# Kernel tuning notes

Measured on AMD Instinct MI355X. Metric: run time of the kernel, lower is better.

The kernel has to match this reference:

```python
import jax, jax.numpy as jnp
import numpy as np

EPS_NORM = 1e-12
EPS_ENT = 1e-12
TEMPERATURE = 0.5
CONTRAST_DENOM = 128.0 * 100.0


def _l2_normalize(x, axis=-1):
    n = jnp.linalg.norm(x, axis=axis, keepdims=True)
    return x / jnp.maximum(n, EPS_NORM)


def setup_inputs() -> dict:
    key0 = jax.random.key(0)
    k1, k2, k3, k4 = jax.random.split(key0, 4)
    B, L, C = 16, 2048, 512
    M = 512
    return {
        "key": jax.random.normal(k1, (B, L, C), dtype=jnp.float32),
        "query": jax.random.normal(k2, (B, L, C), dtype=jnp.float32),
        "keys": jax.random.uniform(k3, (M, C), dtype=jnp.float32),
        "values": jax.random.uniform(k4, (M, C), dtype=jnp.float32),
        "mode": 0,
    }


def reference(key, query, keys, values, mode):
    B, L, C = key.shape
    k = _l2_normalize(key.reshape(-1, C))    # [T, C]
    q = _l2_normalize(query.reshape(-1, C))  # [T, C]

    # --- gatheringLoss ---
    score = jnp.einsum('tc,mc->tm', k, keys)            # [T, M]
    # top-1 of softmax(score) == argmax(score) (softmax is monotone)
    idx = jnp.argmax(score, axis=1)                     # [T]
    nearest_values = values[idx]                        # [T, C]
    gathering_loss = jnp.mean((q - nearest_values) ** 2)

    logits = score / TEMPERATURE                        # [T, M]
    logp = jax.nn.log_softmax(logits, axis=-1)
    gathered = jnp.take_along_axis(logp, idx[:, None], axis=1)  # [T, 1]
    contrast_loss = jnp.sum(gathered) / (-CONTRAST_DENOM)

    # --- read ---
    weights = jax.nn.softmax(score, axis=-1)            # [T, M]
    # EntropyLoss: mean over rows of -sum(w * log(w + eps))
    entropy_loss = jnp.mean(-jnp.sum(weights * jnp.log(weights + EPS_ENT), axis=-1))
    read_query = weights @ values                       # [T, C]

    return (read_query.reshape(B, L, C), entropy_loss, gathering_loss,
            contrast_loss, keys, values)
```

## Files before the change

### kernel.cpp

```cpp
#include <hip/hip_runtime.h>

typedef short short8 __attribute__((ext_vector_type(8)));
typedef float floatx4 __attribute__((ext_vector_type(4)));

#define C_DIM 512
#define KQ_STRIDE 1040
#define ROWS 128

__device__ __forceinline__ unsigned short f2bf(float f) {
    unsigned u = __builtin_bit_cast(unsigned, f);
    u = u + 0x7fffu + ((u >> 16) & 1u);
    return (unsigned short)(u >> 16);
}

__device__ __forceinline__ unsigned skey(float s, int col) {
    unsigned u = __builtin_bit_cast(unsigned, s);
    u = ((int)u < 0) ? ~u : (u | 0x80000000u);
    return (u & ~0x1FFu) | (unsigned)(511 - col);
}

template <int CTRL>
__device__ __forceinline__ float dppAddF(float x) {
    int t = __builtin_amdgcn_update_dpp(0, __builtin_bit_cast(int, x), CTRL, 0xF, 0xF, true);
    return x + __builtin_bit_cast(float, t);
}
template <int CTRL>
__device__ __forceinline__ unsigned dppMaxU(unsigned x) {
    unsigned u = (unsigned)__builtin_amdgcn_update_dpp(0, (int)x, CTRL, 0xF, 0xF, true);
    return u > x ? u : x;
}
__device__ __forceinline__ float rowAdd16(float x) {
    x = dppAddF<0xB1>(x);
    x = dppAddF<0x4E>(x);
    x = dppAddF<0x124>(x);
    x = dppAddF<0x128>(x);
    return x;
}

__global__ __launch_bounds__(256) void pack_kernel(
    const float* __restrict__ keys, const float* __restrict__ values,
    unsigned short* __restrict__ keysFrag, unsigned short* __restrict__ valsFrag,
    float* __restrict__ keysOut, float* __restrict__ valsOut,
    float* __restrict__ scal) {
    int tid = blockIdx.x * 256 + threadIdx.x;
    if (tid < 65536) {
        int e  = tid & 32767;
        int l  = e & 63;
        int NT = (e >> 6) & 31;
        int kt = e >> 11;
        int li = l & 15, q4 = l >> 4;
        unsigned short tmp[8];
        if (tid < 32768) {
            const float* s = keys + (size_t)(NT * 16 + li) * C_DIM + kt * 32 + q4 * 8;
#pragma unroll
            for (int j = 0; j < 8; j++) tmp[j] = f2bf(s[j]);
            unsigned short* d = keysFrag + ((size_t)(kt * 32 + NT) * 64 + l) * 8;
            *(ushort4*)d       = make_ushort4(tmp[0], tmp[1], tmp[2], tmp[3]);
            *(ushort4*)(d + 4) = make_ushort4(tmp[4], tmp[5], tmp[6], tmp[7]);
        } else {
#pragma unroll
            for (int j = 0; j < 8; j++)
                tmp[j] = f2bf(values[(size_t)(kt * 32 + q4 * 8 + j) * C_DIM + NT * 16 + li]);
            unsigned short* d = valsFrag + ((size_t)(kt * 32 + NT) * 64 + l) * 8;
            *(ushort4*)d       = make_ushort4(tmp[0], tmp[1], tmp[2], tmp[3]);
            *(ushort4*)(d + 4) = make_ushort4(tmp[4], tmp[5], tmp[6], tmp[7]);
        }
    } else {
        int ct = tid - 65536;
        if (ct == 0) { scal[0] = 0.f; scal[1] = 0.f; scal[2] = 0.f; }
#pragma unroll
        for (int i = 0; i < 4; i++) {
            int idx = ct + i * 32768;
            if (idx < 65536) ((float4*)keysOut)[idx] = ((const float4*)keys)[idx];
            else             ((float4*)valsOut)[idx - 65536] = ((const float4*)values)[idx - 65536];
        }
    }
}

__global__ __launch_bounds__(512, 2) void fused_kernel(
    const float* __restrict__ key,
    const float* __restrict__ query,
    const unsigned short* __restrict__ keysFrag,
    const unsigned short* __restrict__ valsFrag,
    const float* __restrict__ values,
    float* __restrict__ outRQ,
    float* __restrict__ scal) {
    __shared__ char kq[ROWS * KQ_STRIDE];
    __shared__ __align__(16) float stats[8][ROWS][4];
    __shared__ float gpart[8];

    const int tid = threadIdx.x;
    const int w  = tid >> 6;
    const int l  = tid & 63;
    const int li = l & 15;
    const int q4 = l >> 4;
    const int row0 = blockIdx.x << 7;

    const float* qtb = query + (size_t)row0 * C_DIM;
    float tch0 = qtb[(tid)        * 32];
    float tch1 = qtb[(tid +  512) * 32];
    float tch2 = qtb[(tid + 1024) * 32];
    float tch3 = qtb[(tid + 1536) * 32];

#pragma unroll
    for (int it = 0; it < 4; it++) {
        int r = (w << 4) + (it << 2) + q4;
        const float4* src = (const float4*)(key + (size_t)(row0 + r) * C_DIM);
        float4 v[8];
        float ss = 0.f;
#pragma unroll
        for (int i = 0; i < 8; i++) {
            v[i] = src[i * 16 + li];
            ss += v[i].x * v[i].x + v[i].y * v[i].y + v[i].z * v[i].z + v[i].w * v[i].w;
        }
        ss = rowAdd16(ss);
        float inv = 1.0f / fmaxf(sqrtf(ss), 1e-12f);
        char* dstrow = kq + r * KQ_STRIDE;
#pragma unroll
        for (int i = 0; i < 8; i++) {
            ushort4 b = make_ushort4(f2bf(v[i].x * inv), f2bf(v[i].y * inv),
                                     f2bf(v[i].z * inv), f2bf(v[i].w * inv));
            *(ushort4*)(dstrow + i * 128 + li * 8) = b;
        }
    }
    asm volatile("" :: "v"(tch0), "v"(tch1), "v"(tch2), "v"(tch3));
    __syncthreads();

    floatx4 acc1[32];
#pragma unroll
    for (int i = 0; i < 32; i++) acc1[i] = (floatx4){0.f, 0.f, 0.f, 0.f};
    {
        const short8* kf = (const short8*)keysFrag;
        short8 bcur[4], bnxt[4];
#pragma unroll
        for (int nt = 0; nt < 4; nt++) bcur[nt] = kf[(size_t)((w * 4 + nt) * 64 + l)];
        for (int kt = 0; kt < 16; kt++) {
            if (kt < 15) {
#pragma unroll
                for (int nt = 0; nt < 4; nt++)
                    bnxt[nt] = kf[(size_t)(((kt + 1) * 32 + w * 4 + nt) * 64 + l)];
            }
            short8 a[8];
#pragma unroll
            for (int rg = 0; rg < 8; rg++)
                a[rg] = *(const short8*)(kq + (rg * 16 + li) * KQ_STRIDE + kt * 64 + q4 * 16);
#pragma unroll
            for (int rg = 0; rg < 8; rg++)
#pragma unroll
                for (int nt = 0; nt < 4; nt++)
                    acc1[rg * 4 + nt] = __builtin_amdgcn_mfma_f32_16x16x32_bf16(
                        a[rg], bcur[nt], acc1[rg * 4 + nt], 0, 0, 0);
#pragma unroll
            for (int nt = 0; nt < 4; nt++) bcur[nt] = bnxt[nt];
        }
    }

#pragma unroll
    for (int rg = 0; rg < 8; rg++) {
#pragma unroll
        for (int reg = 0; reg < 4; reg++) {
            const int colbase = (w << 6) + li;
            float s0 = acc1[rg * 4 + 0][reg];
            float s1 = acc1[rg * 4 + 1][reg];
            float s2 = acc1[rg * 4 + 2][reg];
            float s3 = acc1[rg * 4 + 3][reg];
            unsigned K  = skey(s0, colbase);
            unsigned K1 = skey(s1, colbase + 16);
            unsigned K2 = skey(s2, colbase + 32);
            unsigned K3 = skey(s3, colbase + 48);
            K = K1 > K ? K1 : K;
            K = K2 > K ? K2 : K;
            K = K3 > K ? K3 : K;
            float p0 = __expf(s0), p1 = __expf(s1), p2 = __expf(s2), p3 = __expf(s3);
            float z1 = (p0 + p1) + (p2 + p3);
            float e1 = p0 * s0 + p1 * s1 + p2 * s2 + p3 * s3;
            float z2 = p0 * p0 + p1 * p1 + p2 * p2 + p3 * p3;
            acc1[rg * 4 + 0][reg] = p0;
            acc1[rg * 4 + 1][reg] = p1;
            acc1[rg * 4 + 2][reg] = p2;
            acc1[rg * 4 + 3][reg] = p3;
            K = dppMaxU<0xB1>(K);  z1 = dppAddF<0xB1>(z1);  e1 = dppAddF<0xB1>(e1);  z2 = dppAddF<0xB1>(z2);
            K = dppMaxU<0x4E>(K);  z1 = dppAddF<0x4E>(z1);  e1 = dppAddF<0x4E>(e1);  z2 = dppAddF<0x4E>(z2);
            K = dppMaxU<0x124>(K); z1 = dppAddF<0x124>(z1); e1 = dppAddF<0x124>(e1); z2 = dppAddF<0x124>(z2);
            K = dppMaxU<0x128>(K); z1 = dppAddF<0x128>(z1); e1 = dppAddF<0x128>(e1); z2 = dppAddF<0x128>(z2);
            if (li == 0) {
                floatx4 sv;
                sv[0] = __builtin_bit_cast(float, K);
                sv[1] = z1; sv[2] = e1; sv[3] = z2;
                *(floatx4*)stats[w][rg * 16 + q4 * 4 + reg] = sv;
            }
        }
    }
    __syncthreads();

#pragma unroll
    for (int rg = 0; rg < 8; rg++) {
#pragma unroll
        for (int reg = 0; reg < 4; reg++) {
            int r = rg * 16 + q4 * 4 + reg;
#pragma unroll
            for (int nt = 0; nt < 4; nt++) {
                int col = (w << 6) + nt * 16 + li;
                *(unsigned short*)(kq + r * KQ_STRIDE + col * 2) = f2bf(acc1[rg * 4 + nt][reg]);
            }
        }
    }
    __syncthreads();

    floatx4 acc2[32];
#pragma unroll
    for (int i = 0; i < 32; i++) acc2[i] = (floatx4){0.f, 0.f, 0.f, 0.f};
    {
        const short8* vf = (const short8*)valsFrag;
        short8 bcur[4], bnxt[4];
#pragma unroll
        for (int nt = 0; nt < 4; nt++) bcur[nt] = vf[(size_t)((w * 4 + nt) * 64 + l)];
        for (int kt = 0; kt < 16; kt++) {
            if (kt < 15) {
#pragma unroll
                for (int nt = 0; nt < 4; nt++)
                    bnxt[nt] = vf[(size_t)(((kt + 1) * 32 + w * 4 + nt) * 64 + l)];
            }
            short8 a[8];
#pragma unroll
            for (int rg = 0; rg < 8; rg++)
                a[rg] = *(const short8*)(kq + (rg * 16 + li) * KQ_STRIDE + kt * 64 + q4 * 16);
#pragma unroll
            for (int rg = 0; rg < 8; rg++)
#pragma unroll
                for (int nt = 0; nt < 4; nt++)
                    acc2[rg * 4 + nt] = __builtin_amdgcn_mfma_f32_16x16x32_bf16(
                        a[rg], bcur[nt], acc2[rg * 4 + nt], 0, 0, 0);
#pragma unroll
            for (int nt = 0; nt < 4; nt++) bcur[nt] = bnxt[nt];
        }
    }

    unsigned KA, KB; float z1A, e1A, z2A, z1B, e1B, z2B;
    {
        floatx4 vA = *(const floatx4*)stats[0][l];
        floatx4 vB = *(const floatx4*)stats[0][64 + l];
        KA = __builtin_bit_cast(unsigned, vA[0]); z1A = vA[1]; e1A = vA[2]; z2A = vA[3];
        KB = __builtin_bit_cast(unsigned, vB[0]); z1B = vB[1]; e1B = vB[2]; z2B = vB[3];
#pragma unroll
        for (int p = 1; p < 8; p++) {
            floatx4 uA = *(const floatx4*)stats[p][l];
            floatx4 uB = *(const floatx4*)stats[p][64 + l];
            unsigned KoA = __builtin_bit_cast(unsigned, uA[0]);
            unsigned KoB = __builtin_bit_cast(unsigned, uB[0]);
            KA = KoA > KA ? KoA : KA; z1A += uA[1]; e1A += uA[2]; z2A += uA[3];
            KB = KoB > KB ? KoB : KB; z1B += uB[1]; e1B += uB[2]; z2B += uB[3];
        }
    }
    const float izA = 1.0f / z1A;
    const float izB = 1.0f / z1B;
    const int idxA = 511 - (int)(KA & 0x1FFu);
    const int idxB = 511 - (int)(KB & 0x1FFu);

#pragma unroll
    for (int rg = 0; rg < 8; rg++) {
#pragma unroll
        for (int reg = 0; reg < 4; reg++) {
            int r = rg * 16 + q4 * 4 + reg;
            float izr = (rg < 4) ? __shfl(izA, r & 63, 64) : __shfl(izB, r & 63, 64);
            float* orow = outRQ + (size_t)(row0 + r) * C_DIM + (w << 6) + li;
#pragma unroll
            for (int nt = 0; nt < 4; nt++) orow[nt * 16] = acc2[rg * 4 + nt][reg] * izr;
        }
    }

    float gacc = 0.f;
#pragma unroll
    for (int rr = 0; rr < 16; rr++) {
        int r = (w << 4) + rr;
        int idxr = __shfl((w < 4) ? idxA : idxB, r & 63, 64);
        const float4* qr = (const float4*)(query + (size_t)(row0 + r) * C_DIM);
        float4 a = qr[l * 2], b = qr[l * 2 + 1];
        float ss = a.x * a.x + a.y * a.y + a.z * a.z + a.w * a.w +
                   b.x * b.x + b.y * b.y + b.z * b.z + b.w * b.w;
        ss = rowAdd16(ss);
        ss += __shfl_xor(ss, 16, 64);
        ss += __shfl_xor(ss, 32, 64);
        float inv = 1.0f / fmaxf(sqrtf(ss), 1e-12f);
        const float4* vr = (const float4*)(values + (size_t)idxr * C_DIM);
        float4 va = vr[l * 2], vb = vr[l * 2 + 1];
        float d;
        d = a.x * inv - va.x; gacc += d * d;
        d = a.y * inv - va.y; gacc += d * d;
        d = a.z * inv - va.z; gacc += d * d;
        d = a.w * inv - va.w; gacc += d * d;
        d = b.x * inv - vb.x; gacc += d * d;
        d = b.y * inv - vb.y; gacc += d * d;
        d = b.z * inv - vb.z; gacc += d * d;
        d = b.w * inv - vb.w; gacc += d * d;
    }
    gacc = rowAdd16(gacc);
    gacc += __shfl_xor(gacc, 16, 64);
    gacc += __shfl_xor(gacc, 32, 64);
    if (l == 0) gpart[w] = gacc;

    if (w == 0) {
        unsigned umA = (KA >> 31) ? (KA & 0x7FFFFFFFu) : ~KA;
        unsigned umB = (KB >> 31) ? (KB & 0x7FFFFFFFu) : ~KB;
        umA &= ~0x1FFu; umB &= ~0x1FFu;
        float m1A = __builtin_bit_cast(float, umA);
        float m1B = __builtin_bit_cast(float, umB);
        float ent = (__logf(z1A) - e1A * izA) + (__logf(z1B) - e1B * izB);
        float con = (__logf(z2A) - 2.0f * m1A) + (__logf(z2B) - 2.0f * m1B);
#pragma unroll
        for (int msk = 1; msk < 64; msk <<= 1) {
            ent += __shfl_xor(ent, msk, 64);
            con += __shfl_xor(con, msk, 64);
        }
        if (l == 0) {
            atomicAdd(&scal[0], ent * (1.0f / 32768.0f));
            atomicAdd(&scal[2], con * (1.0f / 12800.0f));
        }
    }
    __syncthreads();
    if (tid == 0) {
        float s = 0.f;
#pragma unroll
        for (int i = 0; i < 8; i++) s += gpart[i];
        atomicAdd(&scal[1], s * (1.0f / (32768.0f * 512.0f)));
    }
}

extern "C" void kernel_launch(void* const* d_in, const int* in_sizes, int n_in,
                              void* d_out, int out_size, void* d_ws, size_t ws_size,
                              hipStream_t stream) {
    (void)in_sizes; (void)n_in; (void)out_size; (void)ws_size;
    const float* key    = (const float*)d_in[0];
    const float* query  = (const float*)d_in[1];
    const float* keysIn = (const float*)d_in[2];
    const float* valsIn = (const float*)d_in[3];
    float* out = (float*)d_out;

    unsigned short* keysFrag = (unsigned short*)d_ws;
    unsigned short* valsFrag = keysFrag + 512 * 512;

    float* outRQ   = out;
    float* scal    = out + 16777216;
    float* keysOut = out + 16777219;
    float* valsOut = keysOut + 262144;

    pack_kernel<<<384, 256, 0, stream>>>(keysIn, valsIn, keysFrag, valsFrag,
                                         keysOut, valsOut, scal);
    fused_kernel<<<256, 512, 0, stream>>>(key, query, keysFrag, valsFrag, valsIn, outRQ, scal);
}
```

Baseline: 235.7 us.

## Split fused kernel into score, gather and PV kernels staged through output buffer

Splits the single fused kernel into three launches: a score kernel that writes bf16 probabilities, the per-row inverse sum and the argmax index into scratch space inside the output buffer; a gather kernel that computes the gathering loss; and a PV kernel that reloads the probabilities and does the second matmul. The aim appears to be probing whether the fused kernel's phases (register pressure, serialized query gather) cost more than running them separately. In exchange it adds two launches and a round-trip of the score tile through global memory.

```diff
diff --git a/kernel.cpp b/kernel.cpp
--- a/kernel.cpp
+++ b/kernel.cpp
@@ -77,17 +77,13 @@
     }
 }
 
-__global__ __launch_bounds__(512, 2) void fused_kernel(
+__global__ __launch_bounds__(512, 2) void score_kernel(
     const float* __restrict__ key,
-    const float* __restrict__ query,
     const unsigned short* __restrict__ keysFrag,
-    const unsigned short* __restrict__ valsFrag,
-    const float* __restrict__ values,
     float* __restrict__ outRQ,
     float* __restrict__ scal) {
     __shared__ char kq[ROWS * KQ_STRIDE];
     __shared__ __align__(16) float stats[8][ROWS][4];
-    __shared__ float gpart[8];
 
     const int tid = threadIdx.x;
     const int w  = tid >> 6;
@@ -95,12 +91,7 @@
     const int li = l & 15;
     const int q4 = l >> 4;
     const int row0 = blockIdx.x << 7;
-
-    const float* qtb = query + (size_t)row0 * C_DIM;
-    float tch0 = qtb[(tid)        * 32];
-    float tch1 = qtb[(tid +  512) * 32];
-    float tch2 = qtb[(tid + 1024) * 32];
-    float tch3 = qtb[(tid + 1536) * 32];
+    char* outb = (char*)outRQ;
 
 #pragma unroll
     for (int it = 0; it < 4; it++) {
@@ -123,7 +114,6 @@
             *(ushort4*)(dstrow + i * 128 + li * 8) = b;
         }
     }
-    asm volatile("" :: "v"(tch0), "v"(tch1), "v"(tch2), "v"(tch3));
     __syncthreads();
 
     floatx4 acc1[32];
@@ -193,51 +183,8 @@
     }
     __syncthreads();
 
-#pragma unroll
-    for (int rg = 0; rg < 8; rg++) {
-#pragma unroll
-        for (int reg = 0; reg < 4; reg++) {
-            int r = rg * 16 + q4 * 4 + reg;
-#pragma unroll
-            for (int nt = 0; nt < 4; nt++) {
-                int col = (w << 6) + nt * 16 + li;
-                *(unsigned short*)(kq + r * KQ_STRIDE + col * 2) = f2bf(acc1[rg * 4 + nt][reg]);
-            }
-        }
-    }
-    __syncthreads();
-
-    floatx4 acc2[32];
-#pragma unroll
-    for (int i = 0; i < 32; i++) acc2[i] = (floatx4){0.f, 0.f, 0.f, 0.f};
-    {
-        const short8* vf = (const short8*)valsFrag;
-        short8 bcur[4], bnxt[4];
-#pragma unroll
-        for (int nt = 0; nt < 4; nt++) bcur[nt] = vf[(size_t)((w * 4 + nt) * 64 + l)];
-        for (int kt = 0; kt < 16; kt++) {
-            if (kt < 15) {
-#pragma unroll
-                for (int nt = 0; nt < 4; nt++)
-                    bnxt[nt] = vf[(size_t)(((kt + 1) * 32 + w * 4 + nt) * 64 + l)];
-            }
-            short8 a[8];
-#pragma unroll
-            for (int rg = 0; rg < 8; rg++)
-                a[rg] = *(const short8*)(kq + (rg * 16 + li) * KQ_STRIDE + kt * 64 + q4 * 16);
-#pragma unroll
-            for (int rg = 0; rg < 8; rg++)
-#pragma unroll
-                for (int nt = 0; nt < 4; nt++)
-                    acc2[rg * 4 + nt] = __builtin_amdgcn_mfma_f32_16x16x32_bf16(
-                        a[rg], bcur[nt], acc2[rg * 4 + nt], 0, 0, 0);
-#pragma unroll
-            for (int nt = 0; nt < 4; nt++) bcur[nt] = bnxt[nt];
-        }
-    }
-
-    unsigned KA, KB; float z1A, e1A, z2A, z1B, e1B, z2B;
-    {
+    if (w == 0) {
+        unsigned KA, KB; float z1A, e1A, z2A, z1B, e1B, z2B;
         floatx4 vA = *(const floatx4*)stats[0][l];
         floatx4 vB = *(const floatx4*)stats[0][64 + l];
         KA = __builtin_bit_cast(unsigned, vA[0]); z1A = vA[1]; e1A = vA[2]; z2A = vA[3];
@@ -251,30 +198,71 @@
             KA = KoA > KA ? KoA : KA; z1A += uA[1]; e1A += uA[2]; z2A += uA[3];
             KB = KoB > KB ? KoB : KB; z1B += uB[1]; e1B += uB[2]; z2B += uB[3];
         }
-    }
-    const float izA = 1.0f / z1A;
-    const float izB = 1.0f / z1B;
-    const int idxA = 511 - (int)(KA & 0x1FFu);
-    const int idxB = 511 - (int)(KB & 0x1FFu);
+        float izA = 1.0f / z1A, izB = 1.0f / z1B;
+        int idxA = 511 - (int)(KA & 0x1FFu);
+        int idxB = 511 - (int)(KB & 0x1FFu);
+        char* h0 = outb + (size_t)(row0 + l) * 2048;
+        char* h1 = outb + (size_t)(row0 + 64 + l) * 2048;
+        *(float*)h0 = izA; *(int*)(h0 + 4) = idxA;
+        *(float*)h1 = izB; *(int*)(h1 + 4) = idxB;
+        unsigned umA = (KA >> 31) ? (KA & 0x7FFFFFFFu) : ~KA;
+        unsigned umB = (KB >> 31) ? (KB & 0x7FFFFFFFu) : ~KB;
+        umA &= ~0x1FFu; umB &= ~0x1FFu;
+        float m1A = __builtin_bit_cast(float, umA);
+        float m1B = __builtin_bit_cast(float, umB);
+        float ent = (__logf(z1A) - e1A * izA) + (__logf(z1B) - e1B * izB);
+        float con = (__logf(z2A) - 2.0f * m1A) + (__logf(z2B) - 2.0f * m1B);
+#pragma unroll
+        for (int msk = 1; msk < 64; msk <<= 1) {
+            ent += __shfl_xor(ent, msk, 64);
+            con += __shfl_xor(con, msk, 64);
+        }
+        if (l == 0) {
+            atomicAdd(&scal[0], ent * (1.0f / 32768.0f));
+            atomicAdd(&scal[2], con * (1.0f / 12800.0f));
+        }
+    }
 
 #pragma unroll
     for (int rg = 0; rg < 8; rg++) {
 #pragma unroll
         for (int reg = 0; reg < 4; reg++) {
             int r = rg * 16 + q4 * 4 + reg;
-            float izr = (rg < 4) ? __shfl(izA, r & 63, 64) : __shfl(izB, r & 63, 64);
-            float* orow = outRQ + (size_t)(row0 + r) * C_DIM + (w << 6) + li;
-#pragma unroll
-            for (int nt = 0; nt < 4; nt++) orow[nt * 16] = acc2[rg * 4 + nt][reg] * izr;
-        }
-    }
+#pragma unroll
+            for (int nt = 0; nt < 4; nt++) {
+                int col = (w << 6) + nt * 16 + li;
+                *(unsigned short*)(kq + r * KQ_STRIDE + col * 2) = f2bf(acc1[rg * 4 + nt][reg]);
+            }
+        }
+    }
+    __syncthreads();
+
+#pragma unroll
+    for (int it = 0; it < 16; it++) {
+        int r = (w << 4) + it;
+        float4 t = *(const float4*)(kq + r * KQ_STRIDE + l * 16);
+        *(float4*)(outb + (size_t)(row0 + r) * 2048 + 1024 + l * 16) = t;
+    }
+}
+
+__global__ __launch_bounds__(256) void gather_kernel(
+    const float* __restrict__ query,
+    const float* __restrict__ values,
+    const float* __restrict__ outRQ,
+    float* __restrict__ scal) {
+    __shared__ float gpart[4];
+    const int tid = threadIdx.x;
+    const int w = tid >> 6;
+    const int l = tid & 63;
+    const char* outb = (const char*)outRQ;
+    const int row0 = blockIdx.x * 32;
 
     float gacc = 0.f;
 #pragma unroll
-    for (int rr = 0; rr < 16; rr++) {
-        int r = (w << 4) + rr;
-        int idxr = __shfl((w < 4) ? idxA : idxB, r & 63, 64);
-        const float4* qr = (const float4*)(query + (size_t)(row0 + r) * C_DIM);
+    for (int rr = 0; rr < 8; rr++) {
+        int r = row0 + w * 8 + rr;
+        int idxr = *(const int*)(outb + (size_t)r * 2048 + 4);
+        const float4* qr = (const float4*)(query + (size_t)r * C_DIM);
         float4 a = qr[l * 2], b = qr[l * 2 + 1];
         float ss = a.x * a.x + a.y * a.y + a.z * a.z + a.w * a.w +
                    b.x * b.x + b.y * b.y + b.z * b.z + b.w * b.w;
@@ -298,31 +286,75 @@
     gacc += __shfl_xor(gacc, 16, 64);
     gacc += __shfl_xor(gacc, 32, 64);
     if (l == 0) gpart[w] = gacc;
-
-    if (w == 0) {
-        unsigned umA = (KA >> 31) ? (KA & 0x7FFFFFFFu) : ~KA;
-        unsigned umB = (KB >> 31) ? (KB & 0x7FFFFFFFu) : ~KB;
-        umA &= ~0x1FFu; umB &= ~0x1FFu;
-        float m1A = __builtin_bit_cast(float, umA);
-        float m1B = __builtin_bit_cast(float, umB);
-        float ent = (__logf(z1A) - e1A * izA) + (__logf(z1B) - e1B * izB);
-        float con = (__logf(z2A) - 2.0f * m1A) + (__logf(z2B) - 2.0f * m1B);
-#pragma unroll
-        for (int msk = 1; msk < 64; msk <<= 1) {
-            ent += __shfl_xor(ent, msk, 64);
-            con += __shfl_xor(con, msk, 64);
-        }
-        if (l == 0) {
-            atomicAdd(&scal[0], ent * (1.0f / 32768.0f));
-            atomicAdd(&scal[2], con * (1.0f / 12800.0f));
-        }
-    }
     __syncthreads();
     if (tid == 0) {
-        float s = 0.f;
-#pragma unroll
-        for (int i = 0; i < 8; i++) s += gpart[i];
+        float s = gpart[0] + gpart[1] + gpart[2] + gpart[3];
         atomicAdd(&scal[1], s * (1.0f / (32768.0f * 512.0f)));
+    }
+}
+
+__global__ __launch_bounds__(512, 2) void pv_kernel(
+    const unsigned short* __restrict__ valsFrag,
+    float* __restrict__ outRQ) {
+    __shared__ char kq[ROWS * KQ_STRIDE];
+    __shared__ float izsh[ROWS];
+
+    const int tid = threadIdx.x;
+    const int w  = tid >> 6;
+    const int l  = tid & 63;
+    const int li = l & 15;
+    const int q4 = l >> 4;
+    const int row0 = blockIdx.x << 7;
+    char* outb = (char*)outRQ;
+
+    if (tid < ROWS) izsh[tid] = *(const float*)(outb + (size_t)(row0 + tid) * 2048);
+#pragma unroll
+    for (int it = 0; it < 16; it++) {
+        int r = (w << 4) + it;
+        float4 t = *(const float4*)(outb + (size_t)(row0 + r) * 2048 + 1024 + l * 16);
+        *(float4*)(kq + r * KQ_STRIDE + l * 16) = t;
+    }
+    __syncthreads();
+
+    floatx4 acc2[32];
+#pragma unroll
+    for (int i = 0; i < 32; i++) acc2[i] = (floatx4){0.f, 0.f, 0.f, 0.f};
+    {
+        const short8* vf = (const short8*)valsFrag;
+        short8 bcur[4], bnxt[4];
+#pragma unroll
+        for (int nt = 0; nt < 4; nt++) bcur[nt] = vf[(size_t)((w * 4 + nt) * 64 + l)];
+        for (int kt = 0; kt < 16; kt++) {
+            if (kt < 15) {
+#pragma unroll
+                for (int nt = 0; nt < 4; nt++)
+                    bnxt[nt] = vf[(size_t)(((kt + 1) * 32 + w * 4 + nt) * 64 + l)];
+            }
+            short8 a[8];
+#pragma unroll
+            for (int rg = 0; rg < 8; rg++)
+                a[rg] = *(const short8*)(kq + (rg * 16 + li) * KQ_STRIDE + kt * 64 + q4 * 16);
+#pragma unroll
+            for (int rg = 0; rg < 8; rg++)
+#pragma unroll
+                for (int nt = 0; nt < 4; nt++)
+                    acc2[rg * 4 + nt] = __builtin_amdgcn_mfma_f32_16x16x32_bf16(
+                        a[rg], bcur[nt], acc2[rg * 4 + nt], 0, 0, 0);
+#pragma unroll
+            for (int nt = 0; nt < 4; nt++) bcur[nt] = bnxt[nt];
+        }
+    }
+
+#pragma unroll
+    for (int rg = 0; rg < 8; rg++) {
+#pragma unroll
+        for (int reg = 0; reg < 4; reg++) {
+            int r = rg * 16 + q4 * 4 + reg;
+            float izr = izsh[r];
+            float* orow = outRQ + (size_t)(row0 + r) * C_DIM + (w << 6) + li;
+#pragma unroll
+            for (int nt = 0; nt < 4; nt++) orow[nt * 16] = acc2[rg * 4 + nt][reg] * izr;
+        }
     }
 }
 
@@ -346,5 +378,7 @@
 
     pack_kernel<<<384, 256, 0, stream>>>(keysIn, valsIn, keysFrag, valsFrag,
                                          keysOut, valsOut, scal);
-    fused_kernel<<<256, 512, 0, stream>>>(key, query, keysFrag, valsFrag, valsIn, outRQ, scal);
-}
+    score_kernel<<<256, 512, 0, stream>>>(key, keysFrag, outRQ, scal);
+    gather_kernel<<<1024, 256, 0, stream>>>(query, valsIn, outRQ, scal);
+    pv_kernel<<<256, 512, 0, stream>>>(valsFrag, outRQ);
+}
```

Measured after the change: 234.8 us. No clear change (-0.4%).
